# Optimization experiments

Measured on AMD Instinct MI355X. Metric: run time of the kernel, lower is better.

The kernel has to match this reference:

```python
import jax, jax.numpy as jnp
import numpy as np

B, C_FEAT, H_F, W_F = 16, 256, 80, 80
C_ILL, K, H_Z, W_Z = 64, 3, 40, 40


def setup_inputs() -> dict:
    key = jax.random.key(0)
    k1, k2, k3, k4, k5, k6, k7 = jax.random.split(key, 7)
    feat = jax.random.normal(k1, (B, C_FEAT, H_F, W_F), dtype=jnp.float32)
    Z = jax.random.normal(k2, (B, C_ILL, H_Z, W_Z), dtype=jnp.float32)
    P = jax.random.uniform(k3, (B, K, H_Z, W_Z), dtype=jnp.float32)
    # Expert 1x1-conv params (original zero-inits; use small random for nontrivial math)
    Wg = jax.random.normal(k4, (K, C_FEAT, C_ILL), dtype=jnp.float32) * 0.02
    bg = jax.random.normal(k5, (K, C_FEAT), dtype=jnp.float32) * 0.02
    Wb = jax.random.normal(k6, (K, C_FEAT, C_ILL), dtype=jnp.float32) * 0.02
    bb = jax.random.normal(k7, (K, C_FEAT), dtype=jnp.float32) * 0.02
    return {"feat": feat, "Z": Z, "P": P, "Wg": Wg, "bg": bg, "Wb": Wb, "bb": bb}


def reference(feat, Z, P, Wg, bg, Wb, bb):
    Bb, C, H, W = feat.shape
    # bilinear upsample, half-pixel centers (== torch align_corners=False)
    Z_up = jax.image.resize(Z, (Z.shape[0], Z.shape[1], H, W), method='bilinear')
    P_up = jax.image.resize(P, (P.shape[0], P.shape[1], H, W), method='bilinear')
    # router-weighted illumination features: [B,K,D,H,W]
    ZP = jnp.einsum('bkhw,bdhw->bkdhw', P_up, Z_up)
    # soft-routed 1x1-conv experts, fused across K (weights + router-weighted biases)
    delta_gamma = jnp.einsum('bkdhw,kcd->bchw', ZP, Wg) + jnp.einsum('bkhw,kc->bchw', P_up, bg)
    delta_beta = jnp.einsum('bkdhw,kcd->bchw', ZP, Wb) + jnp.einsum('bkhw,kc->bchw', P_up, bb)
    # FiLM residual modulation
    return feat * (1.0 + delta_gamma) + delta_beta
```

## Files before the change

kernel.cpp:

```cpp
#include <hip/hip_runtime.h>
#include <hip/hip_bf16.h>

#define NB   16
#define NC   256
#define HF   80
#define WF   80
#define NPIX 6400
#define ND   64
#define NK   3
#define HZ   40
#define WZ   40
#define KD   224
#define NKC  7
#define NPB  400
#define ZP_B_STRIDE ((size_t)NPB * NKC * 512)
#define PB_STRIDE   (NKC * 512)
#define A_G_STRIDE  (NKC * 4 * 512)

typedef __bf16 bf16;
typedef __bf16 bf16x8 __attribute__((ext_vector_type(8)));
typedef float  floatx4 __attribute__((ext_vector_type(4)));

__global__ __launch_bounds__(256) void pack_A_kernel(
    const float* __restrict__ Wg, const float* __restrict__ bg,
    const float* __restrict__ Wb, const float* __restrict__ bb,
    bf16* __restrict__ A2)
{
    int i = blockIdx.x * 256 + threadIdx.x;
    int lane = i & 63;
    int j2 = i >> 6;
    int mt = j2 & 3;
    int j3 = j2 >> 2;
    int kc = j3 % 7;
    int g  = j3 / 7;
    int l15 = lane & 15, q = lane >> 4;
    int cbase = (g >> 1) * 64 + (g & 1) * 32;
    int c = cbase + (mt & 1) * 16 + l15;
    const float* W    = (mt >= 2) ? Wb : Wg;
    const float* bias = (mt >= 2) ? bb : bg;
    int kd0 = kc * 32 + q * 8;

    bf16x8 v;
    if (kd0 < NK * ND) {
        int k = kd0 >> 6, d = kd0 & 63;
        const float* src = W + ((size_t)k * NC + c) * ND + d;
        #pragma unroll
        for (int j = 0; j < 8; ++j) v[j] = (bf16)src[j];
    } else if (kd0 == NK * ND) {
        #pragma unroll
        for (int j = 0; j < 8; ++j) v[j] = (bf16)0.0f;
        v[0] = (bf16)bias[0 * NC + c];
        v[1] = (bf16)bias[1 * NC + c];
        v[2] = (bf16)bias[2 * NC + c];
    } else {
        #pragma unroll
        for (int j = 0; j < 8; ++j) v[j] = (bf16)0.0f;
    }
    *reinterpret_cast<bf16x8*>(A2 + (size_t)i * 8) = v;
}

__global__ __launch_bounds__(256) void build_zp_kernel(
    const float* __restrict__ Z, const float* __restrict__ P,
    bf16* __restrict__ ZP2)
{
    __shared__ float z_up[WF][ND + 1];
    __shared__ float p_up[WF][NK];

    const int bid = blockIdx.x;
    const int b   = bid / HF;
    const int h   = bid - b * HF;
    const int t   = threadIdx.x;

    float srch = 0.5f * (float)h - 0.25f;
    float flh  = floorf(srch);
    float fh   = srch - flh;
    int h0 = (int)flh, h1 = h0 + 1;
    h0 = max(h0, 0); h1 = min(h1, HZ - 1);

    #pragma unroll 4
    for (int i = 0; i < 20; ++i) {
        int e = t + 256 * i;
        int d = e / WF;
        int w = e - d * WF;
        float srcw = 0.5f * (float)w - 0.25f;
        float flw  = floorf(srcw);
        float fw   = srcw - flw;
        int w0 = (int)flw, w1 = w0 + 1;
        w0 = max(w0, 0); w1 = min(w1, WZ - 1);
        const float* Zr = Z + (size_t)(b * ND + d) * (HZ * WZ);
        float z00 = Zr[h0 * WZ + w0], z01 = Zr[h0 * WZ + w1];
        float z10 = Zr[h1 * WZ + w0], z11 = Zr[h1 * WZ + w1];
        float zi0 = z00 + fw * (z01 - z00);
        float zi1 = z10 + fw * (z11 - z10);
        z_up[w][d] = zi0 + fh * (zi1 - zi0);
    }
    if (t < WF * NK) {
        int w = t / NK;
        int k = t - w * NK;
        float srcw = 0.5f * (float)w - 0.25f;
        float flw  = floorf(srcw);
        float fw   = srcw - flw;
        int w0 = (int)flw, w1 = w0 + 1;
        w0 = max(w0, 0); w1 = min(w1, WZ - 1);
        const float* Pr = P + (size_t)(b * NK + k) * (HZ * WZ);
        float p00 = Pr[h0 * WZ + w0], p01 = Pr[h0 * WZ + w1];
        float p10 = Pr[h1 * WZ + w0], p11 = Pr[h1 * WZ + w1];
        float pi0 = p00 + fw * (p01 - p00);
        float pi1 = p10 + fw * (p11 - p10);
        p_up[w][k] = pi0 + fh * (pi1 - pi0);
    }
    __syncthreads();

    const size_t rowbase = (size_t)(b * (NPB * NKC) + h * 5 * NKC) * 512;
    for (int i = t; i < 5 * NKC * 64; i += 256) {
        int lane = i & 63;
        int j2   = i >> 6;
        int kc   = j2 % NKC;
        int pb_l = j2 / NKC;
        int l15 = lane & 15, q = lane >> 4;
        int w   = pb_l * 16 + l15;
        int kd0 = kc * 32 + q * 8;
        bf16x8 v;
        if (kd0 < NK * ND) {
            int k  = kd0 >> 6;
            int d0 = kd0 & 63;
            float p = p_up[w][k];
            #pragma unroll
            for (int j = 0; j < 8; ++j)
                v[j] = (bf16)(p * z_up[w][d0 + j]);
        } else if (kd0 == NK * ND) {
            #pragma unroll
            for (int j = 0; j < 8; ++j) v[j] = (bf16)0.0f;
            v[0] = (bf16)p_up[w][0];
            v[1] = (bf16)p_up[w][1];
            v[2] = (bf16)p_up[w][2];
        } else {
            #pragma unroll
            for (int j = 0; j < 8; ++j) v[j] = (bf16)0.0f;
        }
        *reinterpret_cast<bf16x8*>(ZP2 + rowbase + ((size_t)(pb_l * NKC + kc) * 64 + lane) * 8) = v;
    }
}

__global__ __launch_bounds__(256) void gemm_film_kernel(
    const bf16* __restrict__ A2, const bf16* __restrict__ ZP2,
    const float* __restrict__ feat, float* __restrict__ out)
{
    const int ntb = blockIdx.x;
    const int ct  = blockIdx.y;
    const int b   = blockIdx.z;
    const int tid  = threadIdx.x;
    const int lane = tid & 63;
    const int wv   = tid >> 6;
    const int mq   = wv & 1;
    const int nh   = wv >> 1;
    const int l15  = lane & 15;
    const int q    = lane >> 4;

    const int g     = ct * 2 + mq;
    const int cbase = ct * 64 + mq * 32;
    const int pb0   = ntb * 8 + nh * 4;
    const int pix0  = pb0 * 16;

    const bf16* aptr = A2 + (size_t)g * A_G_STRIDE + (size_t)lane * 8;
    const bf16* bptr = ZP2 + (size_t)b * ZP_B_STRIDE + (size_t)pb0 * PB_STRIDE
                       + (size_t)lane * 8;

    floatx4 acc[4][4] = {};

    for (int kc = 0; kc < NKC; ++kc) {
        bf16x8 af[4], bfr[4];
        #pragma unroll
        for (int mt = 0; mt < 4; ++mt)
            af[mt] = *reinterpret_cast<const bf16x8*>(aptr + mt * 512);
        #pragma unroll
        for (int nt = 0; nt < 4; ++nt)
            bfr[nt] = *reinterpret_cast<const bf16x8*>(bptr + nt * PB_STRIDE);
        aptr += 4 * 512;
        bptr += 512;
        #pragma unroll
        for (int mt = 0; mt < 4; ++mt)
            #pragma unroll
            for (int nt = 0; nt < 4; ++nt)
                acc[mt][nt] = __builtin_amdgcn_mfma_f32_16x16x32_bf16(
                    af[mt], bfr[nt], acc[mt][nt], 0, 0, 0);
    }

    const float* featb = feat + (size_t)b * NC * NPIX;
    float* outb = out + (size_t)b * NC * NPIX;
    #pragma unroll
    for (int mt = 0; mt < 2; ++mt) {
        #pragma unroll
        for (int r = 0; r < 4; ++r) {
            int c = cbase + mt * 16 + q * 4 + r;
            const float* frow = featb + (size_t)c * NPIX;
            float* orow = outb + (size_t)c * NPIX;
            #pragma unroll
            for (int nt = 0; nt < 4; ++nt) {
                int pix = pix0 + nt * 16 + l15;
                float gaccum = acc[mt][nt][r];
                float be     = acc[mt + 2][nt][r];
                float f      = frow[pix];
                orow[pix] = f * (1.0f + gaccum) + be;
            }
        }
    }
}

extern "C" void kernel_launch(void* const* d_in, const int* in_sizes, int n_in,
                              void* d_out, int out_size, void* d_ws, size_t ws_size,
                              hipStream_t stream)
{
    (void)in_sizes; (void)n_in; (void)out_size; (void)ws_size;
    const float* feat = (const float*)d_in[0];
    const float* Z    = (const float*)d_in[1];
    const float* P    = (const float*)d_in[2];
    const float* Wg   = (const float*)d_in[3];
    const float* bg   = (const float*)d_in[4];
    const float* Wb   = (const float*)d_in[5];
    const float* bb   = (const float*)d_in[6];

    bf16* ZPw = (bf16*)d_ws;
    bf16* Apk = ZPw + (size_t)NB * ZP_B_STRIDE;
    float* out = (float*)d_out;

    pack_A_kernel<<<56, 256, 0, stream>>>(Wg, bg, Wb, bb, Apk);
    build_zp_kernel<<<NB * HF, 256, 0, stream>>>(Z, P, ZPw);

    dim3 grid(NPIX / 128, NC / 64, NB);
    gemm_film_kernel<<<grid, 256, 0, stream>>>(Apk, ZPw, feat, out);
}
```

Before: 282.0 us.

## Fuse router-weighted ZP construction into GEMM, storing only upsampled Z and P

The prepass no longer materializes the K-expanded bf16 ZP operand (3x64 plus bias chunk per pixel). It writes the upsampled Z in fp32 and the upsampled P separately. The GEMM kernel loads these once per tile and forms the P*Z bf16 B fragments in registers for each K chunk, including the bias row. It also software-pipelines the A fragment loads two chunks ahead and adds a min-waves launch bound. This cuts intermediate write and read traffic, at the cost of more register pressure and in-loop conversion ALU work.

Result: faster. 241.5 us (-14.4%).

```diff
diff --git a/kernel.cpp b/kernel.cpp
--- a/kernel.cpp
+++ b/kernel.cpp
@@ -8,14 +8,10 @@
 #define NPIX 6400
 #define ND   64
 #define NK   3
-#define HZ   40
-#define WZ   40
-#define KD   224
 #define NKC  7
 #define NPB  400
-#define ZP_B_STRIDE ((size_t)NPB * NKC * 512)
-#define PB_STRIDE   (NKC * 512)
 #define A_G_STRIDE  (NKC * 4 * 512)
+
 
 typedef __bf16 bf16;
 typedef __bf16 bf16x8 __attribute__((ext_vector_type(8)));
@@ -59,9 +55,9 @@
     *reinterpret_cast<bf16x8*>(A2 + (size_t)i * 8) = v;
 }
 
-__global__ __launch_bounds__(256) void build_zp_kernel(
+__global__ __launch_bounds__(256) void build_z_kernel(
     const float* __restrict__ Z, const float* __restrict__ P,
-    bf16* __restrict__ ZP2)
+    float* __restrict__ ZF, float* __restrict__ PU)
 {
     __shared__ float z_up[WF][ND + 1];
     __shared__ float p_up[WF][NK];
@@ -75,7 +71,7 @@
     float flh  = floorf(srch);
     float fh   = srch - flh;
     int h0 = (int)flh, h1 = h0 + 1;
-    h0 = max(h0, 0); h1 = min(h1, HZ - 1);
+    h0 = max(h0, 0); h1 = min(h1, 40 - 1);
 
     #pragma unroll 4
     for (int i = 0; i < 20; ++i) {
@@ -86,10 +82,10 @@
         float flw  = floorf(srcw);
         float fw   = srcw - flw;
         int w0 = (int)flw, w1 = w0 + 1;
-        w0 = max(w0, 0); w1 = min(w1, WZ - 1);
-        const float* Zr = Z + (size_t)(b * ND + d) * (HZ * WZ);
-        float z00 = Zr[h0 * WZ + w0], z01 = Zr[h0 * WZ + w1];
-        float z10 = Zr[h1 * WZ + w0], z11 = Zr[h1 * WZ + w1];
+        w0 = max(w0, 0); w1 = min(w1, 40 - 1);
+        const float* Zr = Z + (size_t)(b * ND + d) * (40 * 40);
+        float z00 = Zr[h0 * 40 + w0], z01 = Zr[h0 * 40 + w1];
+        float z10 = Zr[h1 * 40 + w0], z11 = Zr[h1 * 40 + w1];
         float zi0 = z00 + fw * (z01 - z00);
         float zi1 = z10 + fw * (z11 - z10);
         z_up[w][d] = zi0 + fh * (zi1 - zi0);
@@ -101,49 +97,43 @@
         float flw  = floorf(srcw);
         float fw   = srcw - flw;
         int w0 = (int)flw, w1 = w0 + 1;
-        w0 = max(w0, 0); w1 = min(w1, WZ - 1);
-        const float* Pr = P + (size_t)(b * NK + k) * (HZ * WZ);
-        float p00 = Pr[h0 * WZ + w0], p01 = Pr[h0 * WZ + w1];
-        float p10 = Pr[h1 * WZ + w0], p11 = Pr[h1 * WZ + w1];
+        w0 = max(w0, 0); w1 = min(w1, 40 - 1);
+        const float* Pr = P + (size_t)(b * NK + k) * (40 * 40);
+        float p00 = Pr[h0 * 40 + w0], p01 = Pr[h0 * 40 + w1];
+        float p10 = Pr[h1 * 40 + w0], p11 = Pr[h1 * 40 + w1];
         float pi0 = p00 + fw * (p01 - p00);
         float pi1 = p10 + fw * (p11 - p10);
         p_up[w][k] = pi0 + fh * (pi1 - pi0);
     }
     __syncthreads();
 
-    const size_t rowbase = (size_t)(b * (NPB * NKC) + h * 5 * NKC) * 512;
-    for (int i = t; i < 5 * NKC * 64; i += 256) {
+    for (int i = t; i < 640; i += 256) {
         int lane = i & 63;
         int j2   = i >> 6;
-        int kc   = j2 % NKC;
-        int pb_l = j2 / NKC;
+        int half = j2 & 1;
+        int pb_l = j2 >> 1;
         int l15 = lane & 15, q = lane >> 4;
         int w   = pb_l * 16 + l15;
-        int kd0 = kc * 32 + q * 8;
-        bf16x8 v;
-        if (kd0 < NK * ND) {
-            int k  = kd0 >> 6;
-            int d0 = kd0 & 63;
-            float p = p_up[w][k];
-            #pragma unroll
-            for (int j = 0; j < 8; ++j)
-                v[j] = (bf16)(p * z_up[w][d0 + j]);
-        } else if (kd0 == NK * ND) {
-            #pragma unroll
-            for (int j = 0; j < 8; ++j) v[j] = (bf16)0.0f;
-            v[0] = (bf16)p_up[w][0];
-            v[1] = (bf16)p_up[w][1];
-            v[2] = (bf16)p_up[w][2];
-        } else {
-            #pragma unroll
-            for (int j = 0; j < 8; ++j) v[j] = (bf16)0.0f;
-        }
-        *reinterpret_cast<bf16x8*>(ZP2 + rowbase + ((size_t)(pb_l * NKC + kc) * 64 + lane) * 8) = v;
-    }
-}
-
-__global__ __launch_bounds__(256) void gemm_film_kernel(
-    const bf16* __restrict__ A2, const bf16* __restrict__ ZP2,
+        int d0  = half * 32 + q * 8;
+        float* dst = ZF + ((((size_t)(b * NPB + h * 5 + pb_l)) * 2 + half) * 64 + lane) * 8;
+        floatx4 v0, v1;
+        #pragma unroll
+        for (int j = 0; j < 4; ++j) { v0[j] = z_up[w][d0 + j]; v1[j] = z_up[w][d0 + 4 + j]; }
+        *reinterpret_cast<floatx4*>(dst)     = v0;
+        *reinterpret_cast<floatx4*>(dst + 4) = v1;
+    }
+    if (t < 240) {
+        int pb_l = t / 48;
+        int rem  = t - pb_l * 48;
+        int k    = rem >> 4;
+        int l15  = rem & 15;
+        PU[(((size_t)(b * NPB + h * 5 + pb_l)) * 3 + k) * 16 + l15] = p_up[pb_l * 16 + l15][k];
+    }
+}
+
+__global__ __launch_bounds__(256, 2) void gemm_film_kernel(
+    const bf16* __restrict__ A2, const float* __restrict__ ZF,
+    const float* __restrict__ PU,
     const float* __restrict__ feat, float* __restrict__ out)
 {
     const int ntb = blockIdx.x;
@@ -162,28 +152,73 @@
     const int pb0   = ntb * 8 + nh * 4;
     const int pix0  = pb0 * 16;
 
+    floatx4 zf[4][2][2];
+    #pragma unroll
+    for (int nt = 0; nt < 4; ++nt)
+        #pragma unroll
+        for (int hf = 0; hf < 2; ++hf) {
+            const float* cp = ZF + ((((size_t)(b * NPB + pb0 + nt)) * 2 + hf) * 64 + lane) * 8;
+            zf[nt][hf][0] = *reinterpret_cast<const floatx4*>(cp);
+            zf[nt][hf][1] = *reinterpret_cast<const floatx4*>(cp + 4);
+        }
+    float pv[4][3];
+    #pragma unroll
+    for (int nt = 0; nt < 4; ++nt)
+        #pragma unroll
+        for (int k = 0; k < 3; ++k)
+            pv[nt][k] = PU[(((size_t)(b * NPB + pb0 + nt)) * 3 + k) * 16 + l15];
+
     const bf16* aptr = A2 + (size_t)g * A_G_STRIDE + (size_t)lane * 8;
-    const bf16* bptr = ZP2 + (size_t)b * ZP_B_STRIDE + (size_t)pb0 * PB_STRIDE
-                       + (size_t)lane * 8;
+    bf16x8 aA[4], aB[4];
+    #pragma unroll
+    for (int mt = 0; mt < 4; ++mt)
+        aA[mt] = *reinterpret_cast<const bf16x8*>(aptr + mt * 512);
+    #pragma unroll
+    for (int mt = 0; mt < 4; ++mt)
+        aB[mt] = *reinterpret_cast<const bf16x8*>(aptr + 2048 + mt * 512);
 
     floatx4 acc[4][4] = {};
 
+    #pragma unroll
     for (int kc = 0; kc < NKC; ++kc) {
-        bf16x8 af[4], bfr[4];
-        #pragma unroll
-        for (int mt = 0; mt < 4; ++mt)
-            af[mt] = *reinterpret_cast<const bf16x8*>(aptr + mt * 512);
-        #pragma unroll
-        for (int nt = 0; nt < 4; ++nt)
-            bfr[nt] = *reinterpret_cast<const bf16x8*>(bptr + nt * PB_STRIDE);
-        aptr += 4 * 512;
-        bptr += 512;
+        bf16x8 bfr[4];
+        if (kc < 6) {
+            const int hf = kc & 1;
+            const int k  = kc >> 1;
+            #pragma unroll
+            for (int nt = 0; nt < 4; ++nt) {
+                float p = pv[nt][k];
+                #pragma unroll
+                for (int j = 0; j < 4; ++j) {
+                    bfr[nt][j]     = (bf16)(p * zf[nt][hf][0][j]);
+                    bfr[nt][j + 4] = (bf16)(p * zf[nt][hf][1][j]);
+                }
+            }
+        } else {
+            #pragma unroll
+            for (int nt = 0; nt < 4; ++nt) {
+                #pragma unroll
+                for (int j = 0; j < 8; ++j) bfr[nt][j] = (bf16)0.0f;
+                if (q == 0) {
+                    bfr[nt][0] = (bf16)pv[nt][0];
+                    bfr[nt][1] = (bf16)pv[nt][1];
+                    bfr[nt][2] = (bf16)pv[nt][2];
+                }
+            }
+        }
         #pragma unroll
         for (int mt = 0; mt < 4; ++mt)
             #pragma unroll
             for (int nt = 0; nt < 4; ++nt)
                 acc[mt][nt] = __builtin_amdgcn_mfma_f32_16x16x32_bf16(
-                    af[mt], bfr[nt], acc[mt][nt], 0, 0, 0);
+                    aA[mt], bfr[nt], acc[mt][nt], 0, 0, 0);
+        #pragma unroll
+        for (int mt = 0; mt < 4; ++mt) aA[mt] = aB[mt];
+        if (kc + 2 < NKC) {
+            #pragma unroll
+            for (int mt = 0; mt < 4; ++mt)
+                aB[mt] = *reinterpret_cast<const bf16x8*>(aptr + (kc + 2) * 2048 + mt * 512);
+        }
     }
 
     const float* featb = feat + (size_t)b * NC * NPIX;
@@ -220,13 +255,14 @@
     const float* Wb   = (const float*)d_in[5];
     const float* bb   = (const float*)d_in[6];
 
-    bf16* ZPw = (bf16*)d_ws;
-    bf16* Apk = ZPw + (size_t)NB * ZP_B_STRIDE;
+    float* ZF = (float*)d_ws;
+    float* PU = ZF + (size_t)NB * NPB * 2 * 64 * 8;
+    bf16*  Apk = (bf16*)(PU + (size_t)NB * NPB * 3 * 16);
     float* out = (float*)d_out;
 
     pack_A_kernel<<<56, 256, 0, stream>>>(Wg, bg, Wb, bb, Apk);
-    build_zp_kernel<<<NB * HF, 256, 0, stream>>>(Z, P, ZPw);
+    build_z_kernel<<<NB * HF, 256, 0, stream>>>(Z, P, ZF, PU);
 
     dim3 grid(NPIX / 128, NC / 64, NB);
-    gemm_film_kernel<<<grid, 256, 0, stream>>>(Apk, ZPw, feat, out);
-}
+    gemm_film_kernel<<<grid, 256, 0, stream>>>(Apk, ZF, PU, feat, out);
+}
```
